# Performance work log

Measured on AMD Instinct MI355X. Metric: run time of the kernel, lower is better.

Reference implementation:

```python
import jax, jax.numpy as jnp
import numpy as np

# instant-NGP hash grid config (hardcoded in the torch module)
L = 8            # n_levels
F = 2            # n_features_per_level
T = 1 << 16      # hash table size per level
N_MIN = 16
B_GROWTH = float(np.exp(np.log(2048.0 / N_MIN) / (L - 1)))
PRIMES = (1, 2654435761, 805459861)  # tcnn spatial hash primes
N_PTS = 2_097_152


def _grid_encode(uvi, table):
    """uvi: [N,3] in [0,1]; table: [L,T,F]. Returns [N, L*F]."""
    feats = []
    for l in range(L):
        scale = N_MIN * (B_GROWTH ** l) - 1.0           # tcnn grid scale
        res = int(np.ceil(scale)) + 1                    # grid resolution
        pos = uvi * jnp.float32(scale) + 0.5
        p0f = jnp.floor(pos)
        w = pos - p0f                                    # [N,3] trilinear fracs
        p0 = p0f.astype(jnp.uint32)
        hashed = res ** 3 > T                            # dense index if grid fits
        acc = jnp.zeros((uvi.shape[0], F), dtype=table.dtype)
        for c in range(8):
            off_np = np.array([(c >> d) & 1 for d in range(3)], dtype=np.uint32)
            corner = p0 + jnp.asarray(off_np)            # [N,3] uint32
            if hashed:
                idx = ((corner[:, 0] * jnp.uint32(PRIMES[0]))
                       ^ (corner[:, 1] * jnp.uint32(PRIMES[1]))
                       ^ (corner[:, 2] * jnp.uint32(PRIMES[2]))) % jnp.uint32(T)
            else:
                idx = (corner[:, 0]
                       + corner[:, 1] * jnp.uint32(res)
                       + corner[:, 2] * jnp.uint32(res * res))
            wc = jnp.prod(jnp.where(off_np == 1, w, 1.0 - w), axis=-1)  # [N]
            acc = acc + table[l, idx] * wc[:, None]      # irregular gather + lerp
        feats.append(acc)
    return jnp.concatenate(feats, axis=-1)               # [N, L*F]


def setup_inputs() -> dict:
    key = jax.random.key(0)
    ks = jax.random.split(key, 5)
    uvi = jax.random.uniform(ks[0], (N_PTS, 3), dtype=jnp.float32)
    # tcnn initializes hash features uniform in [-1e-4, 1e-4]
    table = jax.random.uniform(ks[1], (L, T, F), dtype=jnp.float32,
                               minval=-1e-4, maxval=1e-4)
    W1 = jax.random.normal(ks[2], (L * F, 64), dtype=jnp.float32) / jnp.sqrt(jnp.float32(L * F))
    b1 = jnp.zeros((64,), dtype=jnp.float32)
    W2 = jax.random.normal(ks[3], (64, 1), dtype=jnp.float32) / 8.0
    b2 = jnp.zeros((1,), dtype=jnp.float32)
    return {"uvi": uvi, "table": table, "W1": W1, "b1": b1, "W2": W2, "b2": b2}


def reference(uvi, table, W1, b1, W2, b2):
    enc = _grid_encode(uvi, table)                       # [N,16]
    h = jax.nn.relu(enc @ W1 + b1)                       # [N,64]
    mask = jax.nn.sigmoid(h @ W2 + b2)                   # [N,1]
    return mask
```

## Files before the change

kernel.cpp:

```cpp
#include <hip/hip_runtime.h>
#include <cmath>
#include <cstdint>

namespace {

constexpr int kLevels = 8;
constexpr uint32_t kT = 1u << 16;
constexpr uint32_t kPrime1 = 2654435761u;
constexpr uint32_t kPrime2 = 805459861u;

struct LevelParams {
    float scale[kLevels];
    uint32_t res[kLevels];
    uint32_t hashed_mask;
};

__global__ __launch_bounds__(256) void ngp_mask_kernel(
    const float* __restrict__ uvi,
    const float* __restrict__ table,
    const float* __restrict__ W1,
    const float* __restrict__ b1,
    const float* __restrict__ W2,
    const float* __restrict__ b2,
    float* __restrict__ out,
    int n, LevelParams lp)
{
    const int i = blockIdx.x * blockDim.x + threadIdx.x;
    if (i >= n) return;

    const float ux = uvi[3 * i + 0];
    const float uy = uvi[3 * i + 1];
    const float uz = uvi[3 * i + 2];

    const float2* __restrict__ tb = reinterpret_cast<const float2*>(table);

    float enc[2 * kLevels];

    #pragma unroll
    for (int l = 0; l < kLevels; ++l) {
        const float s = lp.scale[l];
        const float posx = __fadd_rn(__fmul_rn(ux, s), 0.5f);
        const float posy = __fadd_rn(__fmul_rn(uy, s), 0.5f);
        const float posz = __fadd_rn(__fmul_rn(uz, s), 0.5f);
        const float fx = floorf(posx), fy = floorf(posy), fz = floorf(posz);
        const float wx = __fsub_rn(posx, fx);
        const float wy = __fsub_rn(posy, fy);
        const float wz = __fsub_rn(posz, fz);
        const uint32_t x0 = (uint32_t)fx, y0 = (uint32_t)fy, z0 = (uint32_t)fz;

        const bool hashed = (lp.hashed_mask >> l) & 1u;

        uint32_t hx0, hx1, hy0, hy1, hz0, hz1;
        if (hashed) {
            hx0 = x0;             hx1 = x0 + 1u;
            hy0 = y0 * kPrime1;   hy1 = hy0 + kPrime1;
            hz0 = z0 * kPrime2;   hz1 = hz0 + kPrime2;
        } else {
            const uint32_t r  = lp.res[l];
            const uint32_t r2 = r * r;
            hx0 = x0;             hx1 = x0 + 1u;
            hy0 = y0 * r;         hy1 = hy0 + r;
            hz0 = z0 * r2;        hz1 = hz0 + r2;
        }

        const float wx0 = __fsub_rn(1.f, wx);
        const float wy0 = __fsub_rn(1.f, wy);
        const float wz0 = __fsub_rn(1.f, wz);
        const float w00 = __fmul_rn(wx0, wy0);
        const float w10 = __fmul_rn(wx,  wy0);
        const float w01 = __fmul_rn(wx0, wy);
        const float w11 = __fmul_rn(wx,  wy);

        const uint32_t base = (uint32_t)l << 16;
        float a0 = 0.f, a1 = 0.f;

        #pragma unroll
        for (int c = 0; c < 8; ++c) {
            const uint32_t hx = (c & 1) ? hx1 : hx0;
            const uint32_t hy = (c & 2) ? hy1 : hy0;
            const uint32_t hz = (c & 4) ? hz1 : hz0;
            uint32_t idxc;
            if (hashed) idxc = (hx ^ hy ^ hz) & (kT - 1u);
            else        idxc = hx + hy + hz;
            const float wxy = (c & 2) ? ((c & 1) ? w11 : w01)
                                      : ((c & 1) ? w10 : w00);
            const float wcc = __fmul_rn(wxy, (c & 4) ? wz : wz0);
            const float2 t = tb[base + idxc];
            a0 = __fadd_rn(a0, __fmul_rn(t.x, wcc));
            a1 = __fadd_rn(a1, __fmul_rn(t.y, wcc));
        }
        enc[2 * l + 0] = a0;
        enc[2 * l + 1] = a1;
    }

    float logit = b2[0];
    #pragma unroll
    for (int j = 0; j < 64; ++j) {
        float h = b1[j];
        #pragma unroll
        for (int k = 0; k < 16; ++k)
            h = fmaf(enc[k], W1[k * 64 + j], h);
        h = fmaxf(h, 0.f);
        logit = fmaf(h, W2[j], logit);
    }

    out[i] = 1.f / (1.f + __expf(-logit));
}

}

extern "C" void kernel_launch(void* const* d_in, const int* in_sizes, int n_in,
                              void* d_out, int out_size, void* d_ws, size_t ws_size,
                              hipStream_t stream)
{
    const float* uvi   = (const float*)d_in[0];
    const float* table = (const float*)d_in[1];
    const float* W1    = (const float*)d_in[2];
    const float* b1    = (const float*)d_in[3];
    const float* W2    = (const float*)d_in[4];
    const float* b2    = (const float*)d_in[5];
    float* out = (float*)d_out;

    const int n = in_sizes[0] / 3;

    LevelParams lp;
    const double B = exp(log(2048.0 / 16.0) / (double)(kLevels - 1));
    uint32_t mask = 0;
    for (int l = 0; l < kLevels; ++l) {
        const double scale_d = 16.0 * pow(B, (double)l) - 1.0;
        const long long res = (long long)ceil(scale_d) + 1;
        lp.scale[l] = (float)scale_d;
        lp.res[l]   = (uint32_t)res;
        if (res * res * res > (long long)kT) mask |= (1u << l);
    }
    lp.hashed_mask = mask;

    dim3 block(256);
    dim3 grid((unsigned)((n + 255) / 256));
    hipLaunchKernelGGL(ngp_mask_kernel, grid, block, 0, stream,
                       uvi, table, W1, b1, W2, b2, out, n, lp);
}
```

Before: 343.4 us.

## Split hash encoding and MLP into two kernels with bf16-packed intermediate

```diff
diff --git a/kernel.cpp b/kernel.cpp
--- a/kernel.cpp
+++ b/kernel.cpp
@@ -15,14 +15,10 @@
     uint32_t hashed_mask;
 };
 
-__global__ __launch_bounds__(256) void ngp_mask_kernel(
+__global__ void ngp_encode_kernel(
     const float* __restrict__ uvi,
     const float* __restrict__ table,
-    const float* __restrict__ W1,
-    const float* __restrict__ b1,
-    const float* __restrict__ W2,
-    const float* __restrict__ b2,
-    float* __restrict__ out,
+    uint32_t* __restrict__ enc_out,
     int n, LevelParams lp)
 {
     const int i = blockIdx.x * blockDim.x + threadIdx.x;
@@ -34,18 +30,16 @@
 
     const float2* __restrict__ tb = reinterpret_cast<const float2*>(table);
 
-    float enc[2 * kLevels];
+    uint32_t packed[kLevels];
 
     #pragma unroll
     for (int l = 0; l < kLevels; ++l) {
         const float s = lp.scale[l];
-        const float posx = __fadd_rn(__fmul_rn(ux, s), 0.5f);
-        const float posy = __fadd_rn(__fmul_rn(uy, s), 0.5f);
-        const float posz = __fadd_rn(__fmul_rn(uz, s), 0.5f);
-        const float fx = floorf(posx), fy = floorf(posy), fz = floorf(posz);
-        const float wx = __fsub_rn(posx, fx);
-        const float wy = __fsub_rn(posy, fy);
-        const float wz = __fsub_rn(posz, fz);
+        const float px = fmaf(ux, s, 0.5f);
+        const float py = fmaf(uy, s, 0.5f);
+        const float pz = fmaf(uz, s, 0.5f);
+        const float fx = floorf(px), fy = floorf(py), fz = floorf(pz);
+        const float wx = px - fx, wy = py - fy, wz = pz - fz;
         const uint32_t x0 = (uint32_t)fx, y0 = (uint32_t)fy, z0 = (uint32_t)fz;
 
         const bool hashed = (lp.hashed_mask >> l) & 1u;
@@ -63,13 +57,11 @@
             hz0 = z0 * r2;        hz1 = hz0 + r2;
         }
 
-        const float wx0 = __fsub_rn(1.f, wx);
-        const float wy0 = __fsub_rn(1.f, wy);
-        const float wz0 = __fsub_rn(1.f, wz);
-        const float w00 = __fmul_rn(wx0, wy0);
-        const float w10 = __fmul_rn(wx,  wy0);
-        const float w01 = __fmul_rn(wx0, wy);
-        const float w11 = __fmul_rn(wx,  wy);
+        const float wx0 = 1.f - wx, wy0 = 1.f - wy, wz0 = 1.f - wz;
+        const float w00 = wx0 * wy0;
+        const float w10 = wx  * wy0;
+        const float w01 = wx0 * wy;
+        const float w11 = wx  * wy;
 
         const uint32_t base = (uint32_t)l << 16;
         float a0 = 0.f, a1 = 0.f;
@@ -84,13 +76,41 @@
             else        idxc = hx + hy + hz;
             const float wxy = (c & 2) ? ((c & 1) ? w11 : w01)
                                       : ((c & 1) ? w10 : w00);
-            const float wcc = __fmul_rn(wxy, (c & 4) ? wz : wz0);
+            const float wcc = wxy * ((c & 4) ? wz : wz0);
             const float2 t = tb[base + idxc];
-            a0 = __fadd_rn(a0, __fmul_rn(t.x, wcc));
-            a1 = __fadd_rn(a1, __fmul_rn(t.y, wcc));
-        }
-        enc[2 * l + 0] = a0;
-        enc[2 * l + 1] = a1;
+            a0 = fmaf(t.x, wcc, a0);
+            a1 = fmaf(t.y, wcc, a1);
+        }
+        packed[l] = (__float_as_uint(a0) >> 16) |
+                    (__float_as_uint(a1) & 0xFFFF0000u);
+    }
+
+    uint4* __restrict__ eo = reinterpret_cast<uint4*>(enc_out);
+    eo[2 * i + 0] = make_uint4(packed[0], packed[1], packed[2], packed[3]);
+    eo[2 * i + 1] = make_uint4(packed[4], packed[5], packed[6], packed[7]);
+}
+
+__global__ void ngp_mlp_kernel(
+    const uint32_t* __restrict__ enc_in,
+    const float* __restrict__ W1,
+    const float* __restrict__ b1,
+    const float* __restrict__ W2,
+    const float* __restrict__ b2,
+    float* __restrict__ out, int n)
+{
+    const int i = blockIdx.x * blockDim.x + threadIdx.x;
+    if (i >= n) return;
+
+    const uint4* __restrict__ ei = reinterpret_cast<const uint4*>(enc_in);
+    const uint4 e0 = ei[2 * i + 0];
+    const uint4 e1 = ei[2 * i + 1];
+    const uint32_t pw[8] = {e0.x, e0.y, e0.z, e0.w, e1.x, e1.y, e1.z, e1.w};
+
+    float enc[16];
+    #pragma unroll
+    for (int l = 0; l < 8; ++l) {
+        enc[2 * l + 0] = __uint_as_float(pw[l] << 16);
+        enc[2 * l + 1] = __uint_as_float(pw[l] & 0xFFFF0000u);
     }
 
     float logit = b2[0];
@@ -104,6 +124,82 @@
         logit = fmaf(h, W2[j], logit);
     }
 
+    out[i] = 1.f / (1.f + __expf(-logit));
+}
+
+__global__ __launch_bounds__(256) void ngp_fused_kernel(
+    const float* __restrict__ uvi,
+    const float* __restrict__ table,
+    const float* __restrict__ W1,
+    const float* __restrict__ b1,
+    const float* __restrict__ W2,
+    const float* __restrict__ b2,
+    float* __restrict__ out,
+    int n, LevelParams lp)
+{
+    const int i = blockIdx.x * blockDim.x + threadIdx.x;
+    if (i >= n) return;
+
+    const float ux = uvi[3 * i + 0];
+    const float uy = uvi[3 * i + 1];
+    const float uz = uvi[3 * i + 2];
+    const float2* __restrict__ tb = reinterpret_cast<const float2*>(table);
+
+    float enc[2 * kLevels];
+    #pragma unroll
+    for (int l = 0; l < kLevels; ++l) {
+        const float s = lp.scale[l];
+        const float px = fmaf(ux, s, 0.5f);
+        const float py = fmaf(uy, s, 0.5f);
+        const float pz = fmaf(uz, s, 0.5f);
+        const float fx = floorf(px), fy = floorf(py), fz = floorf(pz);
+        const float wx = px - fx, wy = py - fy, wz = pz - fz;
+        const uint32_t x0 = (uint32_t)fx, y0 = (uint32_t)fy, z0 = (uint32_t)fz;
+        const bool hashed = (lp.hashed_mask >> l) & 1u;
+        uint32_t hx0, hx1, hy0, hy1, hz0, hz1;
+        if (hashed) {
+            hx0 = x0;             hx1 = x0 + 1u;
+            hy0 = y0 * kPrime1;   hy1 = hy0 + kPrime1;
+            hz0 = z0 * kPrime2;   hz1 = hz0 + kPrime2;
+        } else {
+            const uint32_t r  = lp.res[l];
+            const uint32_t r2 = r * r;
+            hx0 = x0;             hx1 = x0 + 1u;
+            hy0 = y0 * r;         hy1 = hy0 + r;
+            hz0 = z0 * r2;        hz1 = hz0 + r2;
+        }
+        const float wx0 = 1.f - wx, wy0 = 1.f - wy, wz0 = 1.f - wz;
+        const float w00 = wx0 * wy0, w10 = wx * wy0, w01 = wx0 * wy, w11 = wx * wy;
+        const uint32_t base = (uint32_t)l << 16;
+        float a0 = 0.f, a1 = 0.f;
+        #pragma unroll
+        for (int c = 0; c < 8; ++c) {
+            const uint32_t hx = (c & 1) ? hx1 : hx0;
+            const uint32_t hy = (c & 2) ? hy1 : hy0;
+            const uint32_t hz = (c & 4) ? hz1 : hz0;
+            uint32_t idxc;
+            if (hashed) idxc = (hx ^ hy ^ hz) & (kT - 1u);
+            else        idxc = hx + hy + hz;
+            const float wxy = (c & 2) ? ((c & 1) ? w11 : w01)
+                                      : ((c & 1) ? w10 : w00);
+            const float wcc = wxy * ((c & 4) ? wz : wz0);
+            const float2 t = tb[base + idxc];
+            a0 = fmaf(t.x, wcc, a0);
+            a1 = fmaf(t.y, wcc, a1);
+        }
+        enc[2 * l + 0] = a0;
+        enc[2 * l + 1] = a1;
+    }
+    float logit = b2[0];
+    #pragma unroll
+    for (int j = 0; j < 64; ++j) {
+        float h = b1[j];
+        #pragma unroll
+        for (int k = 0; k < 16; ++k)
+            h = fmaf(enc[k], W1[k * 64 + j], h);
+        h = fmaxf(h, 0.f);
+        logit = fmaf(h, W2[j], logit);
+    }
     out[i] = 1.f / (1.f + __expf(-logit));
 }
 
@@ -135,8 +231,19 @@
     }
     lp.hashed_mask = mask;
 
+    const size_t enc_bytes = (size_t)n * 8u * 4u;
+
     dim3 block(256);
     dim3 grid((unsigned)((n + 255) / 256));
-    hipLaunchKernelGGL(ngp_mask_kernel, grid, block, 0, stream,
-                       uvi, table, W1, b1, W2, b2, out, n, lp);
-}
+
+    if (ws_size >= enc_bytes) {
+        uint32_t* enc = (uint32_t*)d_ws;
+        hipLaunchKernelGGL(ngp_encode_kernel, grid, block, 0, stream,
+                           uvi, table, enc, n, lp);
+        hipLaunchKernelGGL(ngp_mlp_kernel, grid, block, 0, stream,
+                           enc, W1, b1, W2, b2, out, n);
+    } else {
+        hipLaunchKernelGGL(ngp_fused_kernel, grid, block, 0, stream,
+                           uvi, table, W1, b1, W2, b2, out, n, lp);
+    }
+}
```

Result: slower. 599.1 us (+74.5%).
